# Performance work log

Measured on AMD Instinct MI355X. Metric: run time of the kernel, lower is better.

## Reference

```python
import jax, jax.numpy as jnp
import numpy as np

N = 100000   # nodes
E = 1600000  # edges
F_IN, H1, H2, C = 22, 128, 256, 4


def spmm(edge_src, edge_dst, edge_w, X):
    # A @ X where A is sparse (COO): out[d] = sum_{e: dst[e]=d} w[e] * X[src[e]]
    msgs = X[edge_src] * edge_w[:, None]          # [E, F]
    return jax.ops.segment_sum(msgs, edge_dst, num_segments=N)


def setup_inputs() -> dict:
    key = jax.random.key(0)
    ks = jax.random.split(key, 10)
    x = jax.random.normal(ks[0], (N, F_IN), dtype=jnp.float32)
    edge_src = jax.random.randint(ks[1], (E,), 0, N, dtype=jnp.int32)
    edge_dst = jax.random.randint(ks[2], (E,), 0, N, dtype=jnp.int32)
    edge_w = jax.random.uniform(ks[3], (E,), dtype=jnp.float32)
    s1 = 1.0 / np.sqrt(H1)
    s2 = 1.0 / np.sqrt(H2)
    W1 = jax.random.uniform(ks[4], (F_IN, H1), jnp.float32, -s1, s1)
    b1 = jax.random.uniform(ks[5], (H1,), jnp.float32, -s1, s1)
    W2 = jax.random.uniform(ks[6], (H1, H2), jnp.float32, -s2, s2)
    b2 = jax.random.uniform(ks[7], (H2,), jnp.float32, -s2, s2)
    Wm = jax.random.normal(ks[8], (H2, C), dtype=jnp.float32) * 0.05
    bm = jnp.zeros((C,), dtype=jnp.float32)
    return {"x": x, "edge_src": edge_src, "edge_dst": edge_dst, "edge_w": edge_w,
            "W1": W1, "b1": b1, "W2": W2, "b2": b2, "Wm": Wm, "bm": bm}


def reference(x, edge_src, edge_dst, edge_w, W1, b1, W2, b2, Wm, bm):
    # Layer 1: relu(A @ (X @ W1) + b1)
    h = jax.nn.relu(spmm(edge_src, edge_dst, edge_w, x @ W1) + b1)
    # dropout is a no-op in eval mode
    # Layer 2: A @ (h @ W2) + b2
    h = spmm(edge_src, edge_dst, edge_w, h @ W2) + b2
    # MLP head: Linear(256,4) + LogSoftmax(dim=1)
    return jax.nn.log_softmax(h @ Wm + bm, axis=-1)
```

## Files before the change

kernel.cpp:

```cpp
#include <hip/hip_runtime.h>

#define N_NODES 100000
#define N_EDGES 1600000
#define F_IN 22
#define H1 128
#define H2 256
#define C_OUT 4

#define WDEC(q) __uint_as_float(((q) & 0x7fffu) << 16)
#define BFLO(u) __uint_as_float((u) << 16)
#define BFHI(u) __uint_as_float((u) & 0xFFFF0000u)

#define BSHIFT 9
#define NBUCK 196
#define CHUNK 4096
#define NBLK_A 391
#define BCAP 12288
#define BSLACK 3584
#define XB_BLOCKS 4297

typedef __attribute__((ext_vector_type(8))) short bf16x8;
typedef __attribute__((ext_vector_type(4))) float f32x4;

__global__ __launch_bounds__(256) void binA_xb_k(
    const int* __restrict__ esrc, const int* __restrict__ edst,
    const float* __restrict__ ew, int* __restrict__ bcnt,
    uint2* __restrict__ binned,
    const float* __restrict__ x, unsigned* __restrict__ xb)
{
    __shared__ uint2 l_rec[CHUNK];
    __shared__ int l_base[NBUCK];
    __shared__ int l_cnt[NBUCK];
    int t = threadIdx.x;
    int bid = blockIdx.x;

    if (bid >= NBLK_A) {
        int i = (bid - NBLK_A) * 256 + t;
        if (i < N_NODES * 11) {
            int n = i / 11, p = i - n * 11;
            unsigned u0 = __float_as_uint(x[n * F_IN + 2 * p]);
            unsigned u1 = __float_as_uint(x[n * F_IN + 2 * p + 1]);
            u0 = (u0 + 0x7fffu + ((u0 >> 16) & 1u)) >> 16;
            u1 = (u1 + 0x7fffu + ((u1 >> 16) & 1u)) >> 16;
            xb[i] = u0 | (u1 << 16);
        }
        return;
    }

    int e0 = bid * CHUNK;
    int n = min(CHUNK, N_EDGES - e0);

    for (int i = t; i < NBUCK; i += 256) l_cnt[i] = 0;
    __syncthreads();
    for (int i = t; i < n; i += 256) {
        int e = e0 + i;
        int d = edst[e];
        unsigned u = __float_as_uint(ew[e]);
        unsigned bw = (u + 0x7fffu + ((u >> 16) & 1u)) >> 16;
        unsigned rec = ((unsigned)esrc[e] << 15) | bw;
        l_rec[i] = make_uint2(rec, (unsigned)d);
        atomicAdd(&l_cnt[d >> BSHIFT], 1);
    }
    __syncthreads();
    for (int i = t; i < NBUCK; i += 256) {
        int c = l_cnt[i];
        l_base[i] = c ? atomicAdd(&bcnt[i], c) : 0;
    }
    __syncthreads();
    for (int i = t; i < NBUCK; i += 256) l_cnt[i] = 0;
    __syncthreads();
    for (int i = t; i < n; i += 256) {
        uint2 r = l_rec[i];
        int d = (int)r.y;
        int b = d >> BSHIFT;
        int off = l_base[b] + atomicAdd(&l_cnt[b], 1);
        if (off < BCAP)
            binned[(size_t)b * BCAP + off] = make_uint2(r.x, (unsigned)(d & 511));
    }
}

__global__ __launch_bounds__(512) void scanB_wf_k(
    const int* __restrict__ bcnt, int* __restrict__ bbase,
    const float* __restrict__ W2, const float* __restrict__ Wm,
    const float* __restrict__ b2, const float* __restrict__ bm,
    float* __restrict__ Wf, float* __restrict__ bhead)
{
    int t = threadIdx.x;
    if (blockIdx.x == 0) {
        __shared__ int sA[512], sB[512];
        int v = (t < NBUCK) ? ((bcnt[t] + BSLACK + 7) & ~7) : 0;
        sA[t] = v; __syncthreads();
        int* src = sA; int* dst = sB;
        for (int off = 1; off < 512; off <<= 1) {
            dst[t] = src[t] + (t >= off ? src[t - off] : 0);
            __syncthreads();
            int* tmp = src; src = dst; dst = tmp;
        }
        if (t < NBUCK) bbase[t] = (t > 0) ? src[t - 1] : 0;
    } else {
        int k = t >> 2, c = t & 3;
        float acc = 0.f;
        for (int j = 0; j < H2; ++j)
            acc = fmaf(W2[k * H2 + j], Wm[j * C_OUT + c], acc);
        Wf[k * C_OUT + c] = acc;
        if (t < C_OUT) {
            float a = bm[t];
            for (int j = 0; j < H2; ++j)
                a = fmaf(b2[j], Wm[j * C_OUT + t], a);
            bhead[t] = a;
        }
    }
}

__global__ __launch_bounds__(512) void binB_k(
    const uint2* __restrict__ binned, const int* __restrict__ bcnt,
    const int* __restrict__ bbase, int* __restrict__ rowbeg,
    int* __restrict__ rowend, unsigned* __restrict__ rec_s)
{
    __shared__ int l_hist[512];
    __shared__ int sA[512], sB[512];
    __shared__ int l_cur[512];
    __shared__ unsigned l_out[BCAP];
    int b = blockIdx.x;
    int t = threadIdx.x;
    int node0 = b << BSHIFT;
    int base = bbase[b];
    int cnt = min(bcnt[b], BCAP);
    const uint2* reg = binned + (size_t)b * BCAP;

    l_hist[t] = 0;
    __syncthreads();
    for (int i = t; i < cnt; i += 512)
        atomicAdd(&l_hist[reg[i].y], 1);
    __syncthreads();
    int pc = (l_hist[t] + 7) & ~7;
    sA[t] = pc; __syncthreads();
    int* src = sA; int* dst = sB;
    for (int off = 1; off < 512; off <<= 1) {
        dst[t] = src[t] + (t >= off ? src[t - off] : 0);
        __syncthreads();
        int* tmp = src; src = dst; dst = tmp;
    }
    int excl = (t > 0) ? src[t - 1] : 0;
    int ptot = src[511];
    int node = node0 + t;
    if (node < N_NODES) {
        rowbeg[node] = base + excl;
        rowend[node] = base + excl + pc;
    }
    l_cur[t] = excl;
    __syncthreads();
    for (int i = t; i < ptot; i += 512) l_out[i] = 0;
    __syncthreads();
    for (int i = t; i < cnt; i += 512) {
        uint2 r = reg[i];
        int p = atomicAdd(&l_cur[r.y], 1);
        l_out[p] = r.x;
    }
    __syncthreads();
    for (int i = t; i < ptot; i += 512)
        rec_s[base + i] = l_out[i];
}

__global__ __launch_bounds__(256) void agg1_k(
    const unsigned* __restrict__ xb,
    const int* __restrict__ rowbeg,
    const int* __restrict__ rowend,
    const unsigned* __restrict__ rec,
    unsigned* __restrict__ yb)
{
    int tid = threadIdx.x;
    int g = tid >> 5, lane = tid & 31;
    int d = blockIdx.x * 8 + g;
    int beg = rowbeg[d], end = rowend[d];

    int l2 = lane < 22 ? lane : 21;
    int eslot = l2 >= 11;
    int pair = l2 - 11 * eslot;

    float aA0 = 0.f, aA1 = 0.f, aA2 = 0.f, aA3 = 0.f;
    float aB0 = 0.f, aB1 = 0.f, aB2 = 0.f, aB3 = 0.f;
    int j = beg;
    for (; j + 16 <= end; j += 16) {
        const uint4* r4 = (const uint4*)(rec + j + 8 * eslot);
        uint4 qa = r4[0];
        uint4 qb = r4[1];
        unsigned x0 = xb[(size_t)(qa.x >> 15) * 11 + pair];
        unsigned x1 = xb[(size_t)(qa.y >> 15) * 11 + pair];
        unsigned x2 = xb[(size_t)(qa.z >> 15) * 11 + pair];
        unsigned x3 = xb[(size_t)(qa.w >> 15) * 11 + pair];
        unsigned x4 = xb[(size_t)(qb.x >> 15) * 11 + pair];
        unsigned x5 = xb[(size_t)(qb.y >> 15) * 11 + pair];
        unsigned x6 = xb[(size_t)(qb.z >> 15) * 11 + pair];
        unsigned x7 = xb[(size_t)(qb.w >> 15) * 11 + pair];
        float w0 = WDEC(qa.x), w1 = WDEC(qa.y), w2 = WDEC(qa.z), w3 = WDEC(qa.w);
        float w4 = WDEC(qb.x), w5 = WDEC(qb.y), w6 = WDEC(qb.z), w7 = WDEC(qb.w);
        aA0 = fmaf(w0, BFLO(x0), aA0); aB0 = fmaf(w0, BFHI(x0), aB0);
        aA1 = fmaf(w1, BFLO(x1), aA1); aB1 = fmaf(w1, BFHI(x1), aB1);
        aA2 = fmaf(w2, BFLO(x2), aA2); aB2 = fmaf(w2, BFHI(x2), aB2);
        aA3 = fmaf(w3, BFLO(x3), aA3); aB3 = fmaf(w3, BFHI(x3), aB3);
        aA0 = fmaf(w4, BFLO(x4), aA0); aB0 = fmaf(w4, BFHI(x4), aB0);
        aA1 = fmaf(w5, BFLO(x5), aA1); aB1 = fmaf(w5, BFHI(x5), aB1);
        aA2 = fmaf(w6, BFLO(x6), aA2); aB2 = fmaf(w6, BFHI(x6), aB2);
        aA3 = fmaf(w7, BFLO(x7), aA3); aB3 = fmaf(w7, BFHI(x7), aB3);
    }
    if (j < end) {
        const uint4* r4 = (const uint4*)(rec + j + 4 * eslot);
        uint4 q = r4[0];
        unsigned x0 = xb[(size_t)(q.x >> 15) * 11 + pair];
        unsigned x1 = xb[(size_t)(q.y >> 15) * 11 + pair];
        unsigned x2 = xb[(size_t)(q.z >> 15) * 11 + pair];
        unsigned x3 = xb[(size_t)(q.w >> 15) * 11 + pair];
        float w0 = WDEC(q.x), w1 = WDEC(q.y), w2 = WDEC(q.z), w3 = WDEC(q.w);
        aA0 = fmaf(w0, BFLO(x0), aA0); aB0 = fmaf(w0, BFHI(x0), aB0);
        aA1 = fmaf(w1, BFLO(x1), aA1); aB1 = fmaf(w1, BFHI(x1), aB1);
        aA2 = fmaf(w2, BFLO(x2), aA2); aB2 = fmaf(w2, BFHI(x2), aB2);
        aA3 = fmaf(w3, BFLO(x3), aA3); aB3 = fmaf(w3, BFHI(x3), aB3);
    }
    float sA = (aA0 + aA1) + (aA2 + aA3);
    float sB = (aB0 + aB1) + (aB2 + aB3);
    float oA = __shfl(sA, 11 + pair, 32);
    float oB = __shfl(sB, 11 + pair, 32);
    unsigned u = 0;
    if (lane < 11) {
        unsigned ua = __float_as_uint(sA + oA);
        ua = (ua + 0x7fffu + ((ua >> 16) & 1u)) >> 16;
        unsigned ub = __float_as_uint(sB + oB);
        ub = (ub + 0x7fffu + ((ub >> 16) & 1u)) >> 16;
        u = ua | (ub << 16);
    }
    if (lane < 16)
        yb[(size_t)d * 16 + lane] = u;
}

__global__ __launch_bounds__(256) void gemmz_k(
    const unsigned* __restrict__ yb,
    const float* __restrict__ W1,
    const float* __restrict__ b1,
    const float* __restrict__ Wf,
    float4* __restrict__ z)
{
    __shared__ short w1b[8][64][8];
    __shared__ float4 wsf4[H1];
    __shared__ float bs[H1];
    int tid = threadIdx.x;

    for (int idx = tid; idx < 8 * 64 * 8; idx += 256) {
        int b = idx >> 9;
        int r = idx & 511;
        int l = r >> 3, i = r & 7;
        int k = 8 * (l >> 4) + i;
        int col = 16 * b + (l & 15);
        float v = (k < F_IN) ? W1[k * H1 + col] : 0.f;
        unsigned u = __float_as_uint(v);
        u = (u + 0x7fffu + ((u >> 16) & 1u)) >> 16;
        w1b[b][l][i] = (short)u;
    }
    if (tid < H1) { wsf4[tid] = ((const float4*)Wf)[tid]; bs[tid] = b1[tid]; }
    __syncthreads();

    int wid = tid >> 6, lane = tid & 63;
    int node0 = blockIdx.x * 64 + wid * 16;
    if (node0 >= N_NODES) return;
    int row = lane & 15, q = lane >> 4;

    uint4 av = ((const uint4*)yb)[(size_t)(node0 + row) * 4 + q];
    bf16x8 af = *(bf16x8*)&av;

    float zp[4][4];
#pragma unroll
    for (int i = 0; i < 4; ++i)
#pragma unroll
        for (int c = 0; c < 4; ++c) zp[i][c] = 0.f;

#pragma unroll
    for (int b = 0; b < 8; ++b) {
        bf16x8 bf = *(bf16x8*)&w1b[b][lane][0];
        f32x4 c = __builtin_amdgcn_mfma_f32_16x16x32_bf16(
            af, bf, (f32x4){0.f, 0.f, 0.f, 0.f}, 0, 0, 0);
        int col = 16 * b + (lane & 15);
        float bias = bs[col];
        float4 wv = wsf4[col];
#pragma unroll
        for (int i = 0; i < 4; ++i) {
            float v = c[i] + bias;
            v = v > 0.f ? v : 0.f;
            zp[i][0] = fmaf(v, wv.x, zp[i][0]);
            zp[i][1] = fmaf(v, wv.y, zp[i][1]);
            zp[i][2] = fmaf(v, wv.z, zp[i][2]);
            zp[i][3] = fmaf(v, wv.w, zp[i][3]);
        }
    }
#pragma unroll
    for (int mask = 8; mask >= 1; mask >>= 1)
#pragma unroll
        for (int i = 0; i < 4; ++i) {
            zp[i][0] += __shfl_xor(zp[i][0], mask, 64);
            zp[i][1] += __shfl_xor(zp[i][1], mask, 64);
            zp[i][2] += __shfl_xor(zp[i][2], mask, 64);
            zp[i][3] += __shfl_xor(zp[i][3], mask, 64);
        }
    if ((lane & 15) == 0) {
#pragma unroll
        for (int i = 0; i < 4; ++i) {
            int n = node0 + 4 * q + i;
            z[n] = make_float4(zp[i][0], zp[i][1], zp[i][2], zp[i][3]);
        }
    }
}

__global__ __launch_bounds__(256) void agg4_k(
    const float4* __restrict__ z,
    const int* __restrict__ rowbeg,
    const int* __restrict__ rowend,
    const unsigned* __restrict__ rec,
    const float* __restrict__ bhead,
    float* __restrict__ out)
{
    int tid = threadIdx.x;
    int g = tid >> 3, sub = tid & 7;
    int d = blockIdx.x * 32 + g;
    int beg = rowbeg[d], end = rowend[d];

    float4 acc = {0.f, 0.f, 0.f, 0.f};
    for (int j = beg + sub; j < end; j += 8) {
        unsigned r = rec[j];
        float w = WDEC(r);
        float4 v = z[r >> 15];
        acc.x = fmaf(w, v.x, acc.x);
        acc.y = fmaf(w, v.y, acc.y);
        acc.z = fmaf(w, v.z, acc.z);
        acc.w = fmaf(w, v.w, acc.w);
    }
#pragma unroll
    for (int mask = 4; mask >= 1; mask >>= 1) {
        acc.x += __shfl_xor(acc.x, mask, 64);
        acc.y += __shfl_xor(acc.y, mask, 64);
        acc.z += __shfl_xor(acc.z, mask, 64);
        acc.w += __shfl_xor(acc.w, mask, 64);
    }
    if (sub == 0) {
        float l0 = acc.x + bhead[0];
        float l1 = acc.y + bhead[1];
        float l2 = acc.z + bhead[2];
        float l3 = acc.w + bhead[3];
        float mx = fmaxf(fmaxf(l0, l1), fmaxf(l2, l3));
        float s = expf(l0 - mx) + expf(l1 - mx) + expf(l2 - mx) + expf(l3 - mx);
        float lg = mx + logf(s);
        ((float4*)out)[d] = make_float4(l0 - lg, l1 - lg, l2 - lg, l3 - lg);
    }
}

extern "C" void kernel_launch(void* const* d_in, const int* in_sizes, int n_in,
                              void* d_out, int out_size, void* d_ws, size_t ws_size,
                              hipStream_t stream) {
    const float* x    = (const float*)d_in[0];
    const int*   esrc = (const int*)d_in[1];
    const int*   edst = (const int*)d_in[2];
    const float* ew   = (const float*)d_in[3];
    const float* W1   = (const float*)d_in[4];
    const float* b1   = (const float*)d_in[5];
    const float* W2   = (const float*)d_in[6];
    const float* b2   = (const float*)d_in[7];
    const float* Wm   = (const float*)d_in[8];
    const float* bm   = (const float*)d_in[9];
    float* out = (float*)d_out;

    char* ws = (char*)d_ws;
    float4*   z      = (float4*)ws;   ws += (size_t)N_NODES * 16;
    uint2*    binned = (uint2*)ws;    ws += (size_t)NBUCK * BCAP * 8;
    unsigned* rec_s  = (unsigned*)ws; ws += (size_t)(N_EDGES + NBUCK * (BSLACK + 8)) * 4;
    unsigned* xb     = (unsigned*)ws; ws += (size_t)N_NODES * 11 * 4;
    unsigned* yb     = (unsigned*)ws; ws += (size_t)N_NODES * 16 * 4;
    int*      rowbeg = (int*)ws;      ws += (size_t)N_NODES * 4;
    int*      rowend = (int*)ws;      ws += (size_t)N_NODES * 4;
    int*      bcnt   = (int*)ws;      ws += NBUCK * 4;
    int*      bbase  = (int*)ws;      ws += NBUCK * 4;
    float*    Wf     = (float*)ws;    ws += H1 * C_OUT * 4;
    float*    bhead  = (float*)ws;    ws += C_OUT * 4;

    hipMemsetAsync(bcnt, 0, NBUCK * 4, stream);
    binA_xb_k<<<NBLK_A + XB_BLOCKS, 256, 0, stream>>>(
        esrc, edst, ew, bcnt, binned, x, xb);

    scanB_wf_k<<<2, 512, 0, stream>>>(bcnt, bbase, W2, Wm, b2, bm, Wf, bhead);

    binB_k<<<NBUCK, 512, 0, stream>>>(binned, bcnt, bbase, rowbeg, rowend, rec_s);

    agg1_k<<<N_NODES / 8, 256, 0, stream>>>(xb, rowbeg, rowend, rec_s, yb);
    gemmz_k<<<(N_NODES + 63) / 64, 256, 0, stream>>>(yb, W1, b1, Wf, z);

    agg4_k<<<N_NODES / 32, 256, 0, stream>>>(z, rowbeg, rowend, rec_s, bhead, out);
}
```

Measured before the change: 109.8 us.

## Fuse layer-1 aggregation with the W1 MFMA head projection and halve bucket size

The layer-1 sparse aggregation kernel and the dense W1/ReLU/Wf projection kernel become one kernel. Aggregated bf16 rows now stay in shared memory and feed the MFMA directly, so the intermediate yb buffer is never written to or read from global memory and one launch disappears. In exchange, every 16-node block rebuilds the bf16 W1 tile in shared memory and hits an extra barrier, and only one wave of the 512-thread block does the MFMA stage. Buckets also shrink from 512 to 256 nodes, which doubles the number of binning blocks and cuts their shared-memory footprint.

```diff
diff --git a/kernel.cpp b/kernel.cpp
--- a/kernel.cpp
+++ b/kernel.cpp
@@ -11,12 +11,12 @@
 #define BFLO(u) __uint_as_float((u) << 16)
 #define BFHI(u) __uint_as_float((u) & 0xFFFF0000u)
 
-#define BSHIFT 9
-#define NBUCK 196
+#define BSHIFT 8
+#define NBUCK 391
 #define CHUNK 4096
 #define NBLK_A 391
-#define BCAP 12288
-#define BSLACK 3584
+#define BCAP 6656
+#define BSLACK 1792
 #define XB_BLOCKS 4297
 
 typedef __attribute__((ext_vector_type(8))) short bf16x8;
@@ -75,7 +75,7 @@
         int b = d >> BSHIFT;
         int off = l_base[b] + atomicAdd(&l_cnt[b], 1);
         if (off < BCAP)
-            binned[(size_t)b * BCAP + off] = make_uint2(r.x, (unsigned)(d & 511));
+            binned[(size_t)b * BCAP + off] = make_uint2(r.x, (unsigned)(d & 255));
     }
 }
 
@@ -117,9 +117,9 @@
     const int* __restrict__ bbase, int* __restrict__ rowbeg,
     int* __restrict__ rowend, unsigned* __restrict__ rec_s)
 {
-    __shared__ int l_hist[512];
-    __shared__ int sA[512], sB[512];
-    __shared__ int l_cur[512];
+    __shared__ int l_hist[256];
+    __shared__ int sA[256], sB[256];
+    __shared__ int l_cur[256];
     __shared__ unsigned l_out[BCAP];
     int b = blockIdx.x;
     int t = threadIdx.x;
@@ -128,27 +128,33 @@
     int cnt = min(bcnt[b], BCAP);
     const uint2* reg = binned + (size_t)b * BCAP;
 
-    l_hist[t] = 0;
+    if (t < 256) l_hist[t] = 0;
     __syncthreads();
     for (int i = t; i < cnt; i += 512)
         atomicAdd(&l_hist[reg[i].y], 1);
     __syncthreads();
-    int pc = (l_hist[t] + 7) & ~7;
-    sA[t] = pc; __syncthreads();
+    int pc = 0;
+    if (t < 256) {
+        pc = (l_hist[t] + 7) & ~7;
+        sA[t] = pc;
+    }
+    __syncthreads();
     int* src = sA; int* dst = sB;
-    for (int off = 1; off < 512; off <<= 1) {
-        dst[t] = src[t] + (t >= off ? src[t - off] : 0);
+    for (int off = 1; off < 256; off <<= 1) {
+        if (t < 256) dst[t] = src[t] + (t >= off ? src[t - off] : 0);
         __syncthreads();
         int* tmp = src; src = dst; dst = tmp;
     }
-    int excl = (t > 0) ? src[t - 1] : 0;
-    int ptot = src[511];
-    int node = node0 + t;
-    if (node < N_NODES) {
-        rowbeg[node] = base + excl;
-        rowend[node] = base + excl + pc;
-    }
-    l_cur[t] = excl;
+    int ptot = src[255];
+    if (t < 256) {
+        int excl = (t > 0) ? src[t - 1] : 0;
+        int node = node0 + t;
+        if (node < N_NODES) {
+            rowbeg[node] = base + excl;
+            rowend[node] = base + excl + pc;
+        }
+        l_cur[t] = excl;
+    }
     __syncthreads();
     for (int i = t; i < ptot; i += 512) l_out[i] = 0;
     __syncthreads();
@@ -162,16 +168,37 @@
         rec_s[base + i] = l_out[i];
 }
 
-__global__ __launch_bounds__(256) void agg1_k(
+__global__ __launch_bounds__(512) void agg16_k(
     const unsigned* __restrict__ xb,
     const int* __restrict__ rowbeg,
     const int* __restrict__ rowend,
     const unsigned* __restrict__ rec,
-    unsigned* __restrict__ yb)
-{
+    const float* __restrict__ W1,
+    const float* __restrict__ b1,
+    const float* __restrict__ Wf,
+    float4* __restrict__ z)
+{
+    __shared__ short w1b[8][64][8];
+    __shared__ float4 wsf4[H1];
+    __shared__ float bs[H1];
+    __shared__ unsigned ys[16][16];
     int tid = threadIdx.x;
+
+    for (int idx = tid; idx < 8 * 64 * 8; idx += 512) {
+        int b = idx >> 9;
+        int r = idx & 511;
+        int l = r >> 3, i = r & 7;
+        int k = 8 * (l >> 4) + i;
+        int col = 16 * b + (l & 15);
+        float v = (k < F_IN) ? W1[k * H1 + col] : 0.f;
+        unsigned u = __float_as_uint(v);
+        u = (u + 0x7fffu + ((u >> 16) & 1u)) >> 16;
+        w1b[b][l][i] = (short)u;
+    }
+    if (tid < H1) { wsf4[tid] = ((const float4*)Wf)[tid]; bs[tid] = b1[tid]; }
+
     int g = tid >> 5, lane = tid & 31;
-    int d = blockIdx.x * 8 + g;
+    int d = blockIdx.x * 16 + g;
     int beg = rowbeg[d], end = rowend[d];
 
     int l2 = lane < 22 ? lane : 21;
@@ -229,42 +256,14 @@
         ub = (ub + 0x7fffu + ((ub >> 16) & 1u)) >> 16;
         u = ua | (ub << 16);
     }
-    if (lane < 16)
-        yb[(size_t)d * 16 + lane] = u;
-}
-
-__global__ __launch_bounds__(256) void gemmz_k(
-    const unsigned* __restrict__ yb,
-    const float* __restrict__ W1,
-    const float* __restrict__ b1,
-    const float* __restrict__ Wf,
-    float4* __restrict__ z)
-{
-    __shared__ short w1b[8][64][8];
-    __shared__ float4 wsf4[H1];
-    __shared__ float bs[H1];
-    int tid = threadIdx.x;
-
-    for (int idx = tid; idx < 8 * 64 * 8; idx += 256) {
-        int b = idx >> 9;
-        int r = idx & 511;
-        int l = r >> 3, i = r & 7;
-        int k = 8 * (l >> 4) + i;
-        int col = 16 * b + (l & 15);
-        float v = (k < F_IN) ? W1[k * H1 + col] : 0.f;
-        unsigned u = __float_as_uint(v);
-        u = (u + 0x7fffu + ((u >> 16) & 1u)) >> 16;
-        w1b[b][l][i] = (short)u;
-    }
-    if (tid < H1) { wsf4[tid] = ((const float4*)Wf)[tid]; bs[tid] = b1[tid]; }
-    __syncthreads();
-
-    int wid = tid >> 6, lane = tid & 63;
-    int node0 = blockIdx.x * 64 + wid * 16;
-    if (node0 >= N_NODES) return;
-    int row = lane & 15, q = lane >> 4;
-
-    uint4 av = ((const uint4*)yb)[(size_t)(node0 + row) * 4 + q];
+    if (lane < 16) ys[g][lane] = u;
+    __syncthreads();
+
+    if (tid >= 64) return;
+    int wl = tid;
+    int row = wl & 15, q = wl >> 4;
+
+    uint4 av = *(const uint4*)&ys[row][4 * q];
     bf16x8 af = *(bf16x8*)&av;
 
     float zp[4][4];
@@ -275,10 +274,10 @@
 
 #pragma unroll
     for (int b = 0; b < 8; ++b) {
-        bf16x8 bf = *(bf16x8*)&w1b[b][lane][0];
+        bf16x8 bf = *(bf16x8*)&w1b[b][wl][0];
         f32x4 c = __builtin_amdgcn_mfma_f32_16x16x32_bf16(
             af, bf, (f32x4){0.f, 0.f, 0.f, 0.f}, 0, 0, 0);
-        int col = 16 * b + (lane & 15);
+        int col = 16 * b + row;
         float bias = bs[col];
         float4 wv = wsf4[col];
 #pragma unroll
@@ -300,10 +299,10 @@
             zp[i][2] += __shfl_xor(zp[i][2], mask, 64);
             zp[i][3] += __shfl_xor(zp[i][3], mask, 64);
         }
-    if ((lane & 15) == 0) {
+    if (row == 0) {
 #pragma unroll
         for (int i = 0; i < 4; ++i) {
-            int n = node0 + 4 * q + i;
+            int n = blockIdx.x * 16 + 4 * q + i;
             z[n] = make_float4(zp[i][0], zp[i][1], zp[i][2], zp[i][3]);
         }
     }
@@ -371,7 +370,6 @@
     uint2*    binned = (uint2*)ws;    ws += (size_t)NBUCK * BCAP * 8;
     unsigned* rec_s  = (unsigned*)ws; ws += (size_t)(N_EDGES + NBUCK * (BSLACK + 8)) * 4;
     unsigned* xb     = (unsigned*)ws; ws += (size_t)N_NODES * 11 * 4;
-    unsigned* yb     = (unsigned*)ws; ws += (size_t)N_NODES * 16 * 4;
     int*      rowbeg = (int*)ws;      ws += (size_t)N_NODES * 4;
     int*      rowend = (int*)ws;      ws += (size_t)N_NODES * 4;
     int*      bcnt   = (int*)ws;      ws += NBUCK * 4;
@@ -387,8 +385,7 @@
 
     binB_k<<<NBUCK, 512, 0, stream>>>(binned, bcnt, bbase, rowbeg, rowend, rec_s);
 
-    agg1_k<<<N_NODES / 8, 256, 0, stream>>>(xb, rowbeg, rowend, rec_s, yb);
-    gemmz_k<<<(N_NODES + 63) / 64, 256, 0, stream>>>(yb, W1, b1, Wf, z);
+    agg16_k<<<N_NODES / 16, 512, 0, stream>>>(xb, rowbeg, rowend, rec_s, W1, b1, Wf, z);
 
     agg4_k<<<N_NODES / 32, 256, 0, stream>>>(z, rowbeg, rowend, rec_s, bhead, out);
 }
```

New measurement: 122.8 us. +11.9%, slower.
